# Optimization experiments

Measured on AMD Instinct MI355X. Metric: run time of the kernel, lower is better.

The kernel has to match this reference:

```python
import jax, jax.numpy as jnp
import numpy as np

B, T, H, D = 4, 1024, 16, 64


def setup_inputs() -> dict:
    key = jax.random.key(0)
    kq, kk, kwq, kwk = jax.random.split(key, 4)
    q = jax.random.normal(kq, (B, T, H, D), dtype=jnp.float32)
    k = jax.random.normal(kk, (B, T, H, D), dtype=jnp.float32)
    # HedgehogFeatureMap init: eye weight, zero bias; add small noise so grads flow
    Wq = jnp.eye(D, dtype=jnp.float32) + 0.02 * jax.random.normal(kwq, (D, D), dtype=jnp.float32)
    Wk = jnp.eye(D, dtype=jnp.float32) + 0.02 * jax.random.normal(kwk, (D, D), dtype=jnp.float32)
    bq = jnp.zeros((D,), dtype=jnp.float32)
    bk = jnp.zeros((D,), dtype=jnp.float32)
    return {"q": q, "k": k, "Wq": Wq, "bq": bq, "Wk": Wk, "bk": bk}


def _feature_map(x, W, b):
    # nn.Linear(head_dim, head_dim) then cat([exp(y), exp(-y)], -1) -> [..., 2D]
    y = jnp.einsum('bthd,ed->bthe', x, W) + b
    return jnp.concatenate([jnp.exp(y), jnp.exp(-y)], axis=-1)


def reference(q, k, Wq, bq, Wk, bk):
    # true softmax attention map: [B, T, H, T]
    scale = q.shape[-1] ** 0.5
    scores = jnp.einsum('bthd,bThd->bthT', q, k) / scale
    true_attn_map = jax.nn.softmax(scores, axis=-1)
    # predicted quadratic linear attention with hedgehog feature maps
    phi_q = _feature_map(q, Wq, bq)   # [B,T,H,2D]
    phi_k = _feature_map(k, Wk, bk)   # [B,T,H,2D]
    qk = jnp.einsum('bthd,bThd->bthT', phi_q, phi_k)
    pred_attn_map = qk / jnp.sum(qk, axis=-1, keepdims=True)
    return jnp.stack([true_attn_map, pred_attn_map])  # [2,B,T,H,T]
```

## Files before the change

### kernel.cpp

```cpp
#include <hip/hip_runtime.h>

typedef unsigned short u16;
typedef unsigned int u32;
typedef __attribute__((ext_vector_type(8))) short short8;
typedef __attribute__((ext_vector_type(4))) float floatx4;

#define MFMA16(A,B,C) __builtin_amdgcn_mfma_f32_16x16x32_bf16((A),(B),(C),0,0,0)


__device__ __forceinline__ u16 f2bf(float f){
  u32 u = __float_as_uint(f);
  u32 r = (u + 0x7fffu + ((u >> 16) & 1u)) >> 16;
  return (u16)r;
}
__device__ __forceinline__ float bf2f(u16 h){
  return __uint_as_float(((u32)h) << 16);
}
__device__ __forceinline__ short8 ld8(const u16* p){
  return *(const short8*)p;
}

__global__ __launch_bounds__(256) void featmap_kernel(
    const float* __restrict__ q, const float* __restrict__ k,
    const float* __restrict__ Wq, const float* __restrict__ bq,
    const float* __restrict__ Wk, const float* __restrict__ bk,
    u16* __restrict__ qh, u16* __restrict__ ql,
    u16* __restrict__ kh, u16* __restrict__ kl,
    u16* __restrict__ phiq, u16* __restrict__ phik) {
  u32 gid = blockIdx.x * 256u + threadIdx.x;
  bool is_k = gid >= 65536u;
  u32 r = is_k ? (gid - 65536u) : gid;
  const float* __restrict__ x = (is_k ? k : q) + (size_t)r * 64u;
  const float* __restrict__ W = is_k ? Wk : Wq;
  const float* __restrict__ bias = is_k ? bk : bq;
  u32 b = r >> 14, t = (r >> 4) & 1023u, h = r & 15u;
  u32 orow = (b * 16u + h) * 1024u + t;

  float xv[64];
#pragma unroll
  for (int i = 0; i < 16; i++) {
    float4 v = ((const float4*)x)[i];
    xv[4 * i + 0] = v.x; xv[4 * i + 1] = v.y;
    xv[4 * i + 2] = v.z; xv[4 * i + 3] = v.w;
  }

  float scale = is_k ? 1.0f : 0.125f;
  u16* hdst = (is_k ? kh : qh) + (size_t)orow * 64u;
  u16* ldst = (is_k ? kl : ql) + (size_t)orow * 64u;
#pragma unroll
  for (int c = 0; c < 8; c++) {
    u16 hi[8] __attribute__((aligned(16)));
    u16 lo[8] __attribute__((aligned(16)));
#pragma unroll
    for (int j = 0; j < 8; j++) {
      float xs = xv[c * 8 + j] * scale;
      u16 hb = f2bf(xs);
      hi[j] = hb;
      lo[j] = f2bf(xs - bf2f(hb));
    }
    ((uint4*)hdst)[c] = *(const uint4*)hi;
    ((uint4*)ldst)[c] = *(const uint4*)lo;
  }

  u16* pdst = (is_k ? phik : phiq) + (size_t)orow * 128u;
#pragma unroll
  for (int c = 0; c < 4; c++) {
    float accs[16];
#pragma unroll
    for (int i = 0; i < 16; i++) accs[i] = bias[c * 16 + i];
#pragma unroll
    for (int d = 0; d < 64; d++) {
      float xd = xv[d];
#pragma unroll
      for (int i = 0; i < 16; i++) accs[i] += xd * W[(c * 16 + i) * 64 + d];
    }
    u16 pl[16] __attribute__((aligned(16)));
    u16 pm[16] __attribute__((aligned(16)));
#pragma unroll
    for (int i = 0; i < 16; i++) {
      pl[i] = f2bf(__expf(accs[i]));
      pm[i] = f2bf(__expf(-accs[i]));
    }
    ((uint4*)pdst)[2 * c + 0] = ((const uint4*)pl)[0];
    ((uint4*)pdst)[2 * c + 1] = ((const uint4*)pl)[1];
    ((uint4*)(pdst + 64))[2 * c + 0] = ((const uint4*)pm)[0];
    ((uint4*)(pdst + 64))[2 * c + 1] = ((const uint4*)pm)[1];
  }
}

__global__ __launch_bounds__(128) void colsum_kernel(
    const u16* __restrict__ phik, float* __restrict__ colsum) {
  int bh = blockIdx.x;
  int e = threadIdx.x;
  const u16* p = phik + (size_t)bh * 1024u * 128u + e;
  float s = 0.f;
#pragma unroll 8
  for (int t = 0; t < 1024; t++) s += bf2f(p[(size_t)t * 128u]);
  colsum[bh * 128 + e] = s;
}

__global__ __launch_bounds__(256) void ztrue_kernel(
    const u16* __restrict__ qh, const u16* __restrict__ ql,
    const u16* __restrict__ kh, const u16* __restrict__ kl,
    float* __restrict__ ztrue) {
  int bh = blockIdx.x >> 5, strip = blockIdx.x & 31;
  int tid = threadIdx.x, w = tid >> 6, lane = tid & 63, quad = lane >> 4, n16 = lane & 15;
  u32 base = (u32)bh * 1024u;

  short8 aqh[2][2], aql[2][2];
#pragma unroll
  for (int m = 0; m < 2; m++) {
    u32 row = base + strip * 32u + m * 16u + n16;
#pragma unroll
    for (int ks = 0; ks < 2; ks++) {
      aqh[m][ks] = ld8(qh + (size_t)row * 64u + ks * 32u + quad * 8u);
      aql[m][ks] = ld8(ql + (size_t)row * 64u + ks * 32u + quad * 8u);
    }
  }

  float zp[2][4] = {{0.f,0.f,0.f,0.f},{0.f,0.f,0.f,0.f}};
  for (int ct = w * 16; ct < w * 16 + 16; ++ct) {
    u32 col = base + (u32)ct * 16u + n16;
    const u16* kp = kh + (size_t)col * 64u + quad * 8u;
    const u16* lp = kl + (size_t)col * 64u + quad * 8u;
    short8 b0 = ld8(kp), b1 = ld8(kp + 32), c0 = ld8(lp), c1 = ld8(lp + 32);
#pragma unroll
    for (int m = 0; m < 2; m++) {
      floatx4 acc = {0.f, 0.f, 0.f, 0.f};
      acc = MFMA16(aqh[m][0], b0, acc);
      acc = MFMA16(aqh[m][1], b1, acc);
      acc = MFMA16(aqh[m][0], c0, acc);
      acc = MFMA16(aqh[m][1], c1, acc);
      acc = MFMA16(aql[m][0], b0, acc);
      acc = MFMA16(aql[m][1], b1, acc);
#pragma unroll
      for (int r = 0; r < 4; r++) zp[m][r] += __expf(acc[r]);
    }
  }
#pragma unroll
  for (int m = 0; m < 2; m++)
#pragma unroll
    for (int r = 0; r < 4; r++)
#pragma unroll
      for (int off = 1; off < 16; off <<= 1)
        zp[m][r] += __shfl_xor(zp[m][r], off);

  __shared__ float zbuf[4][32];
  if (n16 == 0) {
#pragma unroll
    for (int m = 0; m < 2; m++)
#pragma unroll
      for (int r = 0; r < 4; r++)
        zbuf[w][m * 16 + quad * 4 + r] = zp[m][r];
  }
  __syncthreads();
  if (tid < 32)
    ztrue[base + strip * 32u + tid] =
        zbuf[0][tid] + zbuf[1][tid] + zbuf[2][tid] + zbuf[3][tid];
}

__global__ __launch_bounds__(256) void emit_kernel(
    const u16* __restrict__ qh, const u16* __restrict__ ql,
    const u16* __restrict__ kh, const u16* __restrict__ kl,
    const u16* __restrict__ phiq, const u16* __restrict__ phik,
    const float* __restrict__ colsum, const float* __restrict__ ztrue,
    float* __restrict__ out) {
  int bh = blockIdx.x >> 5, strip = blockIdx.x & 31;
  int tid = threadIdx.x, w = tid >> 6, lane = tid & 63, quad = lane >> 4, n16 = lane & 15;
  u32 base = (u32)bh * 1024u;

  __shared__ float cs[128];
  __shared__ float rz[2][32];
  if (tid < 128) cs[tid] = colsum[bh * 128 + tid];
  __syncthreads();
  if (tid < 32) {
    u32 row = base + strip * 32u + tid;
    float zpd = 0.f;
#pragma unroll 8
    for (int j = 0; j < 128; j++) zpd += bf2f(phiq[(size_t)row * 128u + j]) * cs[j];
    rz[1][tid] = 1.f / zpd;
    rz[0][tid] = 1.f / ztrue[row];
  }

  short8 aqh[2][2], aql[2][2], apq[2][4];
#pragma unroll
  for (int m = 0; m < 2; m++) {
    u32 row = base + strip * 32u + m * 16u + n16;
#pragma unroll
    for (int ks = 0; ks < 2; ks++) {
      aqh[m][ks] = ld8(qh + (size_t)row * 64u + ks * 32u + quad * 8u);
      aql[m][ks] = ld8(ql + (size_t)row * 64u + ks * 32u + quad * 8u);
    }
#pragma unroll
    for (int ks = 0; ks < 4; ks++)
      apq[m][ks] = ld8(phiq + (size_t)row * 128u + ks * 32u + quad * 8u);
  }
  __syncthreads();

  float rzt[2][4], rzp[2][4];
  u32 tb[2][4];
  u32 bb = (u32)bh >> 4, hh = (u32)bh & 15u;
#pragma unroll
  for (int m = 0; m < 2; m++)
#pragma unroll
    for (int r = 0; r < 4; r++) {
      int rr = m * 16 + quad * 4 + r;
      rzt[m][r] = rz[0][rr];
      rzp[m][r] = rz[1][rr];
      u32 t = strip * 32u + rr;
      tb[m][r] = ((bb * 1024u + t) * 16u + hh) * 1024u;
    }

  for (int ct = w * 16; ct < w * 16 + 16; ++ct) {
    u32 col = base + (u32)ct * 16u + n16;
    const u16* kp = kh + (size_t)col * 64u + quad * 8u;
    const u16* lp = kl + (size_t)col * 64u + quad * 8u;
    const u16* pp = phik + (size_t)col * 128u + quad * 8u;
    short8 b0 = ld8(kp), b1 = ld8(kp + 32), c0 = ld8(lp), c1 = ld8(lp + 32);
    short8 p0 = ld8(pp), p1 = ld8(pp + 32), p2 = ld8(pp + 64), p3 = ld8(pp + 96);
    u32 cidx = (u32)ct * 16u + n16;
#pragma unroll
    for (int m = 0; m < 2; m++) {
      floatx4 acc = {0.f, 0.f, 0.f, 0.f};
      acc = MFMA16(aqh[m][0], b0, acc);
      acc = MFMA16(aqh[m][1], b1, acc);
      acc = MFMA16(aqh[m][0], c0, acc);
      acc = MFMA16(aqh[m][1], c1, acc);
      acc = MFMA16(aql[m][0], b0, acc);
      acc = MFMA16(aql[m][1], b1, acc);
      floatx4 ap = {0.f, 0.f, 0.f, 0.f};
      ap = MFMA16(apq[m][0], p0, ap);
      ap = MFMA16(apq[m][1], p1, ap);
      ap = MFMA16(apq[m][2], p2, ap);
      ap = MFMA16(apq[m][3], p3, ap);
#pragma unroll
      for (int r = 0; r < 4; r++) {
        out[tb[m][r] + cidx] = __expf(acc[r]) * rzt[m][r];
        out[67108864u + tb[m][r] + cidx] = ap[r] * rzp[m][r];
      }
    }
  }
}

extern "C" void kernel_launch(void* const* d_in, const int* in_sizes, int n_in,
                              void* d_out, int out_size, void* d_ws, size_t ws_size,
                              hipStream_t stream) {
  const float* q  = (const float*)d_in[0];
  const float* k  = (const float*)d_in[1];
  const float* Wq = (const float*)d_in[2];
  const float* bq = (const float*)d_in[3];
  const float* Wk = (const float*)d_in[4];
  const float* bk = (const float*)d_in[5];
  unsigned char* ws = (unsigned char*)d_ws;
  u16* qh   = (u16*)(ws + (0ull  << 20));
  u16* ql   = (u16*)(ws + (8ull  << 20));
  u16* kh   = (u16*)(ws + (16ull << 20));
  u16* kl   = (u16*)(ws + (24ull << 20));
  u16* phiq = (u16*)(ws + (32ull << 20));
  u16* phik = (u16*)(ws + (48ull << 20));
  float* colsum = (float*)(ws + (64ull << 20));
  float* ztrue  = (float*)(ws + (64ull << 20) + 32768ull);
  float* out = (float*)d_out;

  hipLaunchKernelGGL(featmap_kernel, dim3(512), dim3(256), 0, stream,
                     q, k, Wq, bq, Wk, bk, qh, ql, kh, kl, phiq, phik);
  hipLaunchKernelGGL(colsum_kernel, dim3(64), dim3(128), 0, stream, phik, colsum);
  hipLaunchKernelGGL(ztrue_kernel, dim3(2048), dim3(256), 0, stream,
                     qh, ql, kh, kl, ztrue);
  hipLaunchKernelGGL(emit_kernel, dim3(2048), dim3(256), 0, stream,
                     qh, ql, kh, kl, phiq, phik, colsum, ztrue, out);
}
```

Measured before the change: 929.6 us.

## Fuse softmax denominator pass into emit kernel with register-held exponentials

Merges the separate ztrue pass into the emit kernel. Each block now owns 16 query rows and keeps all exp(scores) for its row in 64 registers, then reduces the row sum in-block and writes normalized values. MFMA operands are swapped so each lane holds four consecutive columns, which allows float4 stores instead of scalar scattered stores. It also parallelizes the phi_q·colsum dot product across the block. This removes a full recomputation of the QK^T scores, at the cost of higher register pressure and halved rows per block (4096 blocks).

```diff
diff --git a/kernel.cpp b/kernel.cpp
--- a/kernel.cpp
+++ b/kernel.cpp
@@ -99,146 +99,97 @@
   colsum[bh * 128 + e] = s;
 }
 
-__global__ __launch_bounds__(256) void ztrue_kernel(
-    const u16* __restrict__ qh, const u16* __restrict__ ql,
-    const u16* __restrict__ kh, const u16* __restrict__ kl,
-    float* __restrict__ ztrue) {
-  int bh = blockIdx.x >> 5, strip = blockIdx.x & 31;
-  int tid = threadIdx.x, w = tid >> 6, lane = tid & 63, quad = lane >> 4, n16 = lane & 15;
-  u32 base = (u32)bh * 1024u;
-
-  short8 aqh[2][2], aql[2][2];
-#pragma unroll
-  for (int m = 0; m < 2; m++) {
-    u32 row = base + strip * 32u + m * 16u + n16;
-#pragma unroll
-    for (int ks = 0; ks < 2; ks++) {
-      aqh[m][ks] = ld8(qh + (size_t)row * 64u + ks * 32u + quad * 8u);
-      aql[m][ks] = ld8(ql + (size_t)row * 64u + ks * 32u + quad * 8u);
-    }
-  }
-
-  float zp[2][4] = {{0.f,0.f,0.f,0.f},{0.f,0.f,0.f,0.f}};
-  for (int ct = w * 16; ct < w * 16 + 16; ++ct) {
-    u32 col = base + (u32)ct * 16u + n16;
-    const u16* kp = kh + (size_t)col * 64u + quad * 8u;
-    const u16* lp = kl + (size_t)col * 64u + quad * 8u;
-    short8 b0 = ld8(kp), b1 = ld8(kp + 32), c0 = ld8(lp), c1 = ld8(lp + 32);
-#pragma unroll
-    for (int m = 0; m < 2; m++) {
-      floatx4 acc = {0.f, 0.f, 0.f, 0.f};
-      acc = MFMA16(aqh[m][0], b0, acc);
-      acc = MFMA16(aqh[m][1], b1, acc);
-      acc = MFMA16(aqh[m][0], c0, acc);
-      acc = MFMA16(aqh[m][1], c1, acc);
-      acc = MFMA16(aql[m][0], b0, acc);
-      acc = MFMA16(aql[m][1], b1, acc);
-#pragma unroll
-      for (int r = 0; r < 4; r++) zp[m][r] += __expf(acc[r]);
-    }
-  }
-#pragma unroll
-  for (int m = 0; m < 2; m++)
-#pragma unroll
-    for (int r = 0; r < 4; r++)
-#pragma unroll
-      for (int off = 1; off < 16; off <<= 1)
-        zp[m][r] += __shfl_xor(zp[m][r], off);
-
-  __shared__ float zbuf[4][32];
-  if (n16 == 0) {
-#pragma unroll
-    for (int m = 0; m < 2; m++)
-#pragma unroll
-      for (int r = 0; r < 4; r++)
-        zbuf[w][m * 16 + quad * 4 + r] = zp[m][r];
-  }
-  __syncthreads();
-  if (tid < 32)
-    ztrue[base + strip * 32u + tid] =
-        zbuf[0][tid] + zbuf[1][tid] + zbuf[2][tid] + zbuf[3][tid];
-}
-
-__global__ __launch_bounds__(256) void emit_kernel(
+__global__ __launch_bounds__(256) void fused_kernel(
     const u16* __restrict__ qh, const u16* __restrict__ ql,
     const u16* __restrict__ kh, const u16* __restrict__ kl,
     const u16* __restrict__ phiq, const u16* __restrict__ phik,
-    const float* __restrict__ colsum, const float* __restrict__ ztrue,
-    float* __restrict__ out) {
-  int bh = blockIdx.x >> 5, strip = blockIdx.x & 31;
+    const float* __restrict__ colsum, float* __restrict__ out) {
+  int bh = blockIdx.x >> 6, strip = blockIdx.x & 63;
   int tid = threadIdx.x, w = tid >> 6, lane = tid & 63, quad = lane >> 4, n16 = lane & 15;
   u32 base = (u32)bh * 1024u;
 
   __shared__ float cs[128];
-  __shared__ float rz[2][32];
+  __shared__ float rzp_s[16];
+  __shared__ float zb[4][16];
+
   if (tid < 128) cs[tid] = colsum[bh * 128 + tid];
   __syncthreads();
-  if (tid < 32) {
-    u32 row = base + strip * 32u + tid;
-    float zpd = 0.f;
-#pragma unroll 8
-    for (int j = 0; j < 128; j++) zpd += bf2f(phiq[(size_t)row * 128u + j]) * cs[j];
-    rz[1][tid] = 1.f / zpd;
-    rz[0][tid] = 1.f / ztrue[row];
-  }
-
-  short8 aqh[2][2], aql[2][2], apq[2][4];
-#pragma unroll
-  for (int m = 0; m < 2; m++) {
-    u32 row = base + strip * 32u + m * 16u + n16;
-#pragma unroll
-    for (int ks = 0; ks < 2; ks++) {
-      aqh[m][ks] = ld8(qh + (size_t)row * 64u + ks * 32u + quad * 8u);
-      aql[m][ks] = ld8(ql + (size_t)row * 64u + ks * 32u + quad * 8u);
-    }
-#pragma unroll
-    for (int ks = 0; ks < 4; ks++)
-      apq[m][ks] = ld8(phiq + (size_t)row * 128u + ks * 32u + quad * 8u);
-  }
+
+  {
+    int row = tid >> 4, seg = tid & 15;
+    u32 grow = base + strip * 16u + (u32)row;
+    short8 v = ld8(phiq + (size_t)grow * 128u + seg * 8);
+    float p = 0.f;
+#pragma unroll
+    for (int j = 0; j < 8; j++) p += bf2f((u16)v[j]) * cs[seg * 8 + j];
+#pragma unroll
+    for (int off = 1; off < 16; off <<= 1) p += __shfl_xor(p, off);
+    if (seg == 0) rzp_s[row] = 1.f / p;
+  }
+
+  u32 qrow = base + strip * 16u + n16;
+  short8 bqh[2], bql[2], bpq[4];
+#pragma unroll
+  for (int ks = 0; ks < 2; ks++) {
+    bqh[ks] = ld8(qh + (size_t)qrow * 64u + ks * 32u + quad * 8u);
+    bql[ks] = ld8(ql + (size_t)qrow * 64u + ks * 32u + quad * 8u);
+  }
+#pragma unroll
+  for (int ks = 0; ks < 4; ks++)
+    bpq[ks] = ld8(phiq + (size_t)qrow * 128u + ks * 32u + quad * 8u);
+
   __syncthreads();
-
-  float rzt[2][4], rzp[2][4];
-  u32 tb[2][4];
+  float rzp = rzp_s[n16];
+
   u32 bb = (u32)bh >> 4, hh = (u32)bh & 15u;
-#pragma unroll
-  for (int m = 0; m < 2; m++)
-#pragma unroll
-    for (int r = 0; r < 4; r++) {
-      int rr = m * 16 + quad * 4 + r;
-      rzt[m][r] = rz[0][rr];
-      rzp[m][r] = rz[1][rr];
-      u32 t = strip * 32u + rr;
-      tb[m][r] = ((bb * 1024u + t) * 16u + hh) * 1024u;
-    }
-
-  for (int ct = w * 16; ct < w * 16 + 16; ++ct) {
-    u32 col = base + (u32)ct * 16u + n16;
+  u32 t = strip * 16u + n16;
+  float* out0 = out + ((size_t)(bb * 1024u + t) * 16u + hh) * 1024u;
+  float* out1 = out0 + 67108864u;
+
+  float pt[64];
+#pragma unroll
+  for (int ct = 0; ct < 16; ct++) {
+    u32 col = base + (u32)(w * 16 + ct) * 16u + n16;
     const u16* kp = kh + (size_t)col * 64u + quad * 8u;
     const u16* lp = kl + (size_t)col * 64u + quad * 8u;
     const u16* pp = phik + (size_t)col * 128u + quad * 8u;
     short8 b0 = ld8(kp), b1 = ld8(kp + 32), c0 = ld8(lp), c1 = ld8(lp + 32);
     short8 p0 = ld8(pp), p1 = ld8(pp + 32), p2 = ld8(pp + 64), p3 = ld8(pp + 96);
-    u32 cidx = (u32)ct * 16u + n16;
-#pragma unroll
-    for (int m = 0; m < 2; m++) {
-      floatx4 acc = {0.f, 0.f, 0.f, 0.f};
-      acc = MFMA16(aqh[m][0], b0, acc);
-      acc = MFMA16(aqh[m][1], b1, acc);
-      acc = MFMA16(aqh[m][0], c0, acc);
-      acc = MFMA16(aqh[m][1], c1, acc);
-      acc = MFMA16(aql[m][0], b0, acc);
-      acc = MFMA16(aql[m][1], b1, acc);
-      floatx4 ap = {0.f, 0.f, 0.f, 0.f};
-      ap = MFMA16(apq[m][0], p0, ap);
-      ap = MFMA16(apq[m][1], p1, ap);
-      ap = MFMA16(apq[m][2], p2, ap);
-      ap = MFMA16(apq[m][3], p3, ap);
-#pragma unroll
-      for (int r = 0; r < 4; r++) {
-        out[tb[m][r] + cidx] = __expf(acc[r]) * rzt[m][r];
-        out[67108864u + tb[m][r] + cidx] = ap[r] * rzp[m][r];
-      }
-    }
+    floatx4 acc = {0.f, 0.f, 0.f, 0.f};
+    acc = MFMA16(b0, bqh[0], acc);
+    acc = MFMA16(b1, bqh[1], acc);
+    acc = MFMA16(c0, bqh[0], acc);
+    acc = MFMA16(c1, bqh[1], acc);
+    acc = MFMA16(b0, bql[0], acc);
+    acc = MFMA16(b1, bql[1], acc);
+    floatx4 ap = {0.f, 0.f, 0.f, 0.f};
+    ap = MFMA16(p0, bpq[0], ap);
+    ap = MFMA16(p1, bpq[1], ap);
+    ap = MFMA16(p2, bpq[2], ap);
+    ap = MFMA16(p3, bpq[3], ap);
+#pragma unroll
+    for (int r = 0; r < 4; r++) pt[ct * 4 + r] = __expf(acc[r]);
+    float4 ov;
+    ov.x = ap[0] * rzp; ov.y = ap[1] * rzp;
+    ov.z = ap[2] * rzp; ov.w = ap[3] * rzp;
+    *(float4*)(out1 + (u32)(w * 16 + ct) * 16u + quad * 4u) = ov;
+  }
+
+  float s = 0.f;
+#pragma unroll
+  for (int i = 0; i < 64; i++) s += pt[i];
+  s += __shfl_xor(s, 16);
+  s += __shfl_xor(s, 32);
+  if (lane < 16) zb[w][lane] = s;
+  __syncthreads();
+  float rzt = 1.f / (zb[0][n16] + zb[1][n16] + zb[2][n16] + zb[3][n16]);
+
+#pragma unroll
+  for (int ct = 0; ct < 16; ct++) {
+    float4 ov;
+    ov.x = pt[ct * 4 + 0] * rzt; ov.y = pt[ct * 4 + 1] * rzt;
+    ov.z = pt[ct * 4 + 2] * rzt; ov.w = pt[ct * 4 + 3] * rzt;
+    *(float4*)(out0 + (u32)(w * 16 + ct) * 16u + quad * 4u) = ov;
   }
 }
 
@@ -259,14 +210,11 @@
   u16* phiq = (u16*)(ws + (32ull << 20));
   u16* phik = (u16*)(ws + (48ull << 20));
   float* colsum = (float*)(ws + (64ull << 20));
-  float* ztrue  = (float*)(ws + (64ull << 20) + 32768ull);
   float* out = (float*)d_out;
 
   hipLaunchKernelGGL(featmap_kernel, dim3(512), dim3(256), 0, stream,
                      q, k, Wq, bq, Wk, bk, qh, ql, kh, kl, phiq, phik);
   hipLaunchKernelGGL(colsum_kernel, dim3(64), dim3(128), 0, stream, phik, colsum);
-  hipLaunchKernelGGL(ztrue_kernel, dim3(2048), dim3(256), 0, stream,
-                     qh, ql, kh, kl, ztrue);
-  hipLaunchKernelGGL(emit_kernel, dim3(2048), dim3(256), 0, stream,
-                     qh, ql, kh, kl, phiq, phik, colsum, ztrue, out);
-}
+  hipLaunchKernelGGL(fused_kernel, dim3(4096), dim3(256), 0, stream,
+                     qh, ql, kh, kl, phiq, phik, colsum, out);
+}
```

Result: no change. 937.6 us (+0.9%).
